# Kernel tuning notes

Hardware: AMD Instinct MI355X
Metric: run time of the kernel (lower is better)

Reference implementation:

```python
import jax, jax.numpy as jnp
import numpy as np

DT = 0.1  # fixed dt offset from init_kwargs


def setup_inputs() -> dict:
    key = jax.random.key(0)
    ks = jax.random.split(key, 8)
    B_, L, D, N = 4, 4096, 128, 16
    s = 1.0 / np.sqrt(D)
    # S4D-Real init: A_n = -(n+1), repeated over input_dim (random_init=False)
    A = jnp.broadcast_to(-(jnp.arange(N, dtype=jnp.float32) + 1.0), (D, N))
    return {
        "x": jax.random.normal(ks[0], (B_, L, D), dtype=jnp.float32),
        "A": A,
        "Wb": jax.random.uniform(ks[1], (N, D), minval=-s, maxval=s, dtype=jnp.float32),
        "bb": jax.random.uniform(ks[2], (N,), minval=-s, maxval=s, dtype=jnp.float32),
        "Wc": jax.random.uniform(ks[3], (N, D), minval=-s, maxval=s, dtype=jnp.float32),
        "bc": jax.random.uniform(ks[4], (N,), minval=-s, maxval=s, dtype=jnp.float32),
        "Wd": jax.random.uniform(ks[5], (1, D), minval=-s, maxval=s, dtype=jnp.float32),
        "bd": jax.random.uniform(ks[6], (1,), minval=-s, maxval=s, dtype=jnp.float32),
    }


def reference(x, A, Wb, bb, Wc, bc, Wd, bd):
    # x: [B, L, D]; A: [D, N]
    Bp = x @ Wb.T + bb                                   # [B, L, N]  (self.sb)
    C = x @ Wc.T + bc                                    # [B, L, N]  (self.sc)
    # DeltaNetwork: softplus(Linear(x)) + dt, repeated over input_dim
    delta = jax.nn.softplus(x @ Wd.T + bd) + DT          # [B, L, 1]
    delta = jnp.broadcast_to(delta, x.shape)             # [B, L, D]
    # discretize: A_bar = exp(dt*A); B_bar = (1 - exp(-dt*A)) * (dt x B)
    dA = delta[..., None] * A                            # [B, L, D, N]
    A_bar = jnp.exp(dA)
    Bx = (1.0 - jnp.exp(-dA)) * delta[..., None] * Bp[:, :, None, :] * x[..., None]  # B_bar * x_t

    def step(h, inp):
        A_t, Bx_t, C_t = inp                             # [B,D,N],[B,D,N],[B,N]
        h = A_t * h + Bx_t
        y_t = jnp.sum(h * C_t[:, None, :], axis=-1)      # [B, D]
        return h, y_t

    h0 = jnp.zeros((x.shape[0], x.shape[2], A.shape[1]), x.dtype)
    _, y = jax.lax.scan(
        step, h0,
        (A_bar.transpose(1, 0, 2, 3), Bx.transpose(1, 0, 2, 3), C.transpose(1, 0, 2)),
    )
    return y.transpose(1, 0, 2)                          # [B, L, D]
```

## Files before the change

kernel.cpp:

```cpp
#include <hip/hip_runtime.h>
#include <math.h>

#define B_ 4
#define L_ 4096
#define D_ 128
#define N_ 16
#define DT_ 0.1f
#define CHUNK_ 32
#define NC_ 128

#define HL_OFF 0
#define H0_OFF 1048576
#define P_OFF  2097152
#define W_OFF  2105344

__global__ __launch_bounds__(256) void kA_fused(const float* __restrict__ x,
                                                const float* __restrict__ A,
                                                const float* __restrict__ Wb,
                                                const float* __restrict__ bb,
                                                const float* __restrict__ Wc,
                                                const float* __restrict__ bc,
                                                const float* __restrict__ Wd,
                                                const float* __restrict__ bd,
                                                float* __restrict__ ws,
                                                float* __restrict__ y) {
    __shared__ float xs[32][132];
    __shared__ float proj[32][34];
    __shared__ float delta_s[32];
    __shared__ float Ssum[32];
    __shared__ float a_s[32][16];
    __shared__ float c_s[32][16];
    __shared__ float C_s[32][16];

    const int t = threadIdx.x;
    const int blk = blockIdx.x;
    const int b = blk >> 7;
    const int c = blk & 127;
    const int l0 = c * CHUNK_;

    const float4* xg = (const float4*)(x + ((size_t)b * L_ + l0) * 128);
#pragma unroll
    for (int i = t; i < 1024; i += 256) {
        float4 v = xg[i];
        int r = i >> 5, c4 = (i & 31) << 2;
        xs[r][c4] = v.x; xs[r][c4 + 1] = v.y;
        xs[r][c4 + 2] = v.z; xs[r][c4 + 3] = v.w;
    }
    __syncthreads();

    {
        const int wv = t >> 6;
        const int lane = t & 63;
        const int r = lane & 31;
        const int oh = lane >> 5;
        const int ob = wv * 8 + oh * 4;
        const float* wp = (ob < 16) ? (Wb + (size_t)ob * 128)
                                    : (Wc + (size_t)(ob - 16) * 128);
        const bool do32 = (wv == 0) && (oh == 0);
        float a0 = 0.f, a1 = 0.f, a2 = 0.f, a3 = 0.f, ad = 0.f;
#pragma unroll 4
        for (int k4 = 0; k4 < 32; ++k4) {
            float4 xv = *(const float4*)&xs[r][k4 * 4];
            float4 w0 = *(const float4*)(wp + k4 * 4);
            float4 w1 = *(const float4*)(wp + 128 + k4 * 4);
            float4 w2 = *(const float4*)(wp + 256 + k4 * 4);
            float4 w3 = *(const float4*)(wp + 384 + k4 * 4);
            a0 = fmaf(xv.x, w0.x, a0); a0 = fmaf(xv.y, w0.y, a0);
            a0 = fmaf(xv.z, w0.z, a0); a0 = fmaf(xv.w, w0.w, a0);
            a1 = fmaf(xv.x, w1.x, a1); a1 = fmaf(xv.y, w1.y, a1);
            a1 = fmaf(xv.z, w1.z, a1); a1 = fmaf(xv.w, w1.w, a1);
            a2 = fmaf(xv.x, w2.x, a2); a2 = fmaf(xv.y, w2.y, a2);
            a2 = fmaf(xv.z, w2.z, a2); a2 = fmaf(xv.w, w2.w, a2);
            a3 = fmaf(xv.x, w3.x, a3); a3 = fmaf(xv.y, w3.y, a3);
            a3 = fmaf(xv.z, w3.z, a3); a3 = fmaf(xv.w, w3.w, a3);
            if (do32) {
                float4 w4 = *(const float4*)(Wd + k4 * 4);
                ad = fmaf(xv.x, w4.x, ad); ad = fmaf(xv.y, w4.y, ad);
                ad = fmaf(xv.z, w4.z, ad); ad = fmaf(xv.w, w4.w, ad);
            }
        }
        proj[r][ob] = a0; proj[r][ob + 1] = a1;
        proj[r][ob + 2] = a2; proj[r][ob + 3] = a3;
        if (do32) proj[r][32] = ad;
    }
    __syncthreads();

    if (t < 32) {
        float z = proj[t][32] + bd[0];
        float sp = fmaxf(z, 0.f) + log1pf(expf(-fabsf(z)));
        delta_s[t] = sp + DT_;
    }
    __syncthreads();
    if (t == 0) {
        float s = 0.f;
        for (int r = 0; r < 32; ++r) { s += delta_s[r]; Ssum[r] = s; }
    }
    __syncthreads();

    {
        float* wglob = ws + W_OFF + ((size_t)b * L_ + l0) * 16;
#pragma unroll
        for (int p = t; p < 512; p += 256) {
            int r = p >> 4, n = p & 15;
            float An = A[n];
            float delta = delta_s[r];
            float Bp = proj[r][n] + bb[n];
            float Cv = proj[r][16 + n] + bc[n];
            float dA = delta * An;
            a_s[r][n] = expf(dA);
            c_s[r][n] = (1.f - expf(-dA)) * delta * Bp;
            C_s[r][n] = Cv;
            wglob[p] = Cv * expf(An * Ssum[r]);
        }
        if (t < 16) {
            ws[P_OFF + (size_t)blk * 16 + t] = expf(A[t] * Ssum[31]);
        }
    }
    __syncthreads();

    const int dd = t >> 2;
    const int nq = t & 3;
    float h0v = 0.f, h1v = 0.f, h2v = 0.f, h3v = 0.f;
    float g0v = 0.f, g1v = 0.f, g2v = 0.f, g3v = 0.f;
    float* yout = y + ((size_t)b * L_ + l0) * 128;
#pragma unroll 4
    for (int tt = 0; tt < 32; ++tt) {
        float4 av = *(const float4*)&a_s[tt][nq * 4];
        float4 cv = *(const float4*)&c_s[tt][nq * 4];
        float4 Cv = *(const float4*)&C_s[tt][nq * 4];
        float x0 = xs[tt][dd];
        float x1 = xs[tt][dd + 64];
        h0v = fmaf(av.x, h0v, cv.x * x0);
        h1v = fmaf(av.y, h1v, cv.y * x0);
        h2v = fmaf(av.z, h2v, cv.z * x0);
        h3v = fmaf(av.w, h3v, cv.w * x0);
        g0v = fmaf(av.x, g0v, cv.x * x1);
        g1v = fmaf(av.y, g1v, cv.y * x1);
        g2v = fmaf(av.z, g2v, cv.z * x1);
        g3v = fmaf(av.w, g3v, cv.w * x1);
        float y0 = h0v * Cv.x;
        y0 = fmaf(h1v, Cv.y, y0); y0 = fmaf(h2v, Cv.z, y0); y0 = fmaf(h3v, Cv.w, y0);
        float y1 = g0v * Cv.x;
        y1 = fmaf(g1v, Cv.y, y1); y1 = fmaf(g2v, Cv.z, y1); y1 = fmaf(g3v, Cv.w, y1);
        y0 += __shfl_xor(y0, 1); y0 += __shfl_xor(y0, 2);
        y1 += __shfl_xor(y1, 1); y1 += __shfl_xor(y1, 2);
        if (nq == 0) {
            yout[tt * 128 + dd] = y0;
            yout[tt * 128 + dd + 64] = y1;
        }
    }
    float* hL = ws + HL_OFF + (size_t)blk * 2048;
    *(float4*)(hL + dd * 16 + nq * 4) = make_float4(h0v, h1v, h2v, h3v);
    *(float4*)(hL + (dd + 64) * 16 + nq * 4) = make_float4(g0v, g1v, g2v, g3v);
}

__global__ __launch_bounds__(256, 4) void kB_combine(float* __restrict__ ws) {
    const float* hL = ws + HL_OFF;
    const float* Pp = ws + P_OFF;
    float* h0 = ws + H0_OFF;
    const int tid = blockIdx.x * 256 + threadIdx.x;
    const int b = tid >> 11;
    const int dn = tid & 2047;
    const int n = tid & 15;

    const float* hp = hL + (size_t)b * NC_ * 2048 + dn;
    const float* pp = Pp + (size_t)b * NC_ * 16 + n;
    float* op = h0 + (size_t)b * NC_ * 2048 + dn;

    float h = 0.f;
    op[0] = 0.f;
#pragma unroll 8
    for (int c = 0; c < NC_ - 1; ++c) {
        float hl = hp[(size_t)c * 2048];
        float p  = pp[(size_t)c * 16];
        h = fmaf(p, h, hl);
        op[(size_t)(c + 1) * 2048] = h;
    }
}

__global__ __launch_bounds__(256, 4) void kC_update(const float* __restrict__ ws,
                                                    float* __restrict__ y) {
    __shared__ float w_s[32][16];
    const int blk = blockIdx.x;
    const int b = blk >> 7;
    const int c = blk & 127;
    const int t = threadIdx.x;

    if (t < 128) {
        float4 v = ((const float4*)(ws + W_OFF + ((size_t)b * L_ + c * CHUNK_) * 16))[t];
        int tt = t >> 2, n0 = (t & 3) << 2;
        w_s[tt][n0] = v.x; w_s[tt][n0 + 1] = v.y;
        w_s[tt][n0 + 2] = v.z; w_s[tt][n0 + 3] = v.w;
    }
    __syncthreads();

    const int d = t & 127;
    const int rh = t >> 7;
    const float* h0p = ws + H0_OFF + ((size_t)blk * 128 + d) * 16;
    const float4 ha = *(const float4*)h0p;
    const float4 hb = *(const float4*)(h0p + 4);
    const float4 hc = *(const float4*)(h0p + 8);
    const float4 hd = *(const float4*)(h0p + 12);

    float* yp = y + ((size_t)b * L_ + c * CHUNK_ + rh * 16) * 128 + d;
#pragma unroll
    for (int i = 0; i < 16; ++i) {
        const int tt = rh * 16 + i;
        float4 wa = *(const float4*)&w_s[tt][0];
        float4 wb4 = *(const float4*)&w_s[tt][4];
        float4 wc4 = *(const float4*)&w_s[tt][8];
        float4 wd4 = *(const float4*)&w_s[tt][12];
        float s = yp[i * 128];
        s = fmaf(wa.x, ha.x, s); s = fmaf(wa.y, ha.y, s);
        s = fmaf(wa.z, ha.z, s); s = fmaf(wa.w, ha.w, s);
        s = fmaf(wb4.x, hb.x, s); s = fmaf(wb4.y, hb.y, s);
        s = fmaf(wb4.z, hb.z, s); s = fmaf(wb4.w, hb.w, s);
        s = fmaf(wc4.x, hc.x, s); s = fmaf(wc4.y, hc.y, s);
        s = fmaf(wc4.z, hc.z, s); s = fmaf(wc4.w, hc.w, s);
        s = fmaf(wd4.x, hd.x, s); s = fmaf(wd4.y, hd.y, s);
        s = fmaf(wd4.z, hd.z, s); s = fmaf(wd4.w, hd.w, s);
        yp[i * 128] = s;
    }
}

extern "C" void kernel_launch(void* const* d_in, const int* in_sizes, int n_in,
                              void* d_out, int out_size, void* d_ws, size_t ws_size,
                              hipStream_t stream) {
    const float* x  = (const float*)d_in[0];
    const float* A  = (const float*)d_in[1];
    const float* Wb = (const float*)d_in[2];
    const float* bb = (const float*)d_in[3];
    const float* Wc = (const float*)d_in[4];
    const float* bc = (const float*)d_in[5];
    const float* Wd = (const float*)d_in[6];
    const float* bd = (const float*)d_in[7];
    float* ws = (float*)d_ws;
    float* y  = (float*)d_out;

    kA_fused<<<512, 256, 0, stream>>>(x, A, Wb, bb, Wc, bc, Wd, bd, ws, y);
    kB_combine<<<32, 256, 0, stream>>>(ws);
    kC_update<<<512, 256, 0, stream>>>(ws, y);
}
```

Measured before the change: 131.2 us.

## Fuse chunked scan into one kernel with inter-block flag sync

```diff
diff --git a/kernel.cpp b/kernel.cpp
--- a/kernel.cpp
+++ b/kernel.cpp
@@ -6,59 +6,56 @@
 #define D_ 128
 #define N_ 16
 #define DT_ 0.1f
-#define CHUNK_ 32
-#define NC_ 128
-
-#define HL_OFF 0
-#define H0_OFF 1048576
-#define P_OFF  2097152
-#define W_OFF  2105344
-
-__global__ __launch_bounds__(256) void kA_fused(const float* __restrict__ x,
-                                                const float* __restrict__ A,
-                                                const float* __restrict__ Wb,
-                                                const float* __restrict__ bb,
-                                                const float* __restrict__ Wc,
-                                                const float* __restrict__ bc,
-                                                const float* __restrict__ Wd,
-                                                const float* __restrict__ bd,
-                                                float* __restrict__ ws,
-                                                float* __restrict__ y) {
-    __shared__ float xs[32][132];
-    __shared__ float proj[32][34];
-    __shared__ float delta_s[32];
-    __shared__ float Ssum[32];
-    __shared__ float a_s[32][16];
-    __shared__ float c_s[32][16];
-    __shared__ float C_s[32][16];
+#define CH_ 64
+#define NCH_ 64
+#define MAGICF 0x5D5D5D5Du
+
+#define CF_OFF 0
+#define HL_OFF 786432
+#define PR_OFF 1310720
+#define FL_OFF 1314816
+
+__global__ __launch_bounds__(512, 2) void s6_fused(const float* __restrict__ x,
+                                                   const float* __restrict__ A,
+                                                   const float* __restrict__ Wb,
+                                                   const float* __restrict__ bb,
+                                                   const float* __restrict__ Wc,
+                                                   const float* __restrict__ bc,
+                                                   const float* __restrict__ Wd,
+                                                   const float* __restrict__ bd,
+                                                   float* __restrict__ ws,
+                                                   float* __restrict__ y) {
+    __shared__ float xs[64][132];
+    __shared__ float proj[64][36];
+    __shared__ float delta_s[64];
+    __shared__ float Ssum[64];
+    __shared__ float w_s[64][16];
+    __shared__ float ylocal[64][132];
+    __shared__ float h0s[128][20];
 
     const int t = threadIdx.x;
     const int blk = blockIdx.x;
-    const int b = blk >> 7;
-    const int c = blk & 127;
-    const int l0 = c * CHUNK_;
-
-    const float4* xg = (const float4*)(x + ((size_t)b * L_ + l0) * 128);
-#pragma unroll
-    for (int i = t; i < 1024; i += 256) {
+    const int b = blk >> 6;
+    const int c = blk & 63;
+    const size_t rowbase = (size_t)b * L_ + c * CH_;
+
+    const float4* xg = (const float4*)(x + rowbase * 128);
+#pragma unroll
+    for (int i = t; i < 2048; i += 512) {
         float4 v = xg[i];
-        int r = i >> 5, c4 = (i & 31) << 2;
-        xs[r][c4] = v.x; xs[r][c4 + 1] = v.y;
-        xs[r][c4 + 2] = v.z; xs[r][c4 + 3] = v.w;
+        int r = i >> 5, k4 = (i & 31) << 2;
+        xs[r][k4] = v.x; xs[r][k4 + 1] = v.y;
+        xs[r][k4 + 2] = v.z; xs[r][k4 + 3] = v.w;
     }
     __syncthreads();
 
     {
-        const int wv = t >> 6;
-        const int lane = t & 63;
-        const int r = lane & 31;
-        const int oh = lane >> 5;
-        const int ob = wv * 8 + oh * 4;
-        const float* wp = (ob < 16) ? (Wb + (size_t)ob * 128)
-                                    : (Wc + (size_t)(ob - 16) * 128);
-        const bool do32 = (wv == 0) && (oh == 0);
-        float a0 = 0.f, a1 = 0.f, a2 = 0.f, a3 = 0.f, ad = 0.f;
-#pragma unroll 4
+        const int q = t >> 6;
+        const int r = t & 63;
+        const float* wp = (q < 4) ? (Wb + (size_t)q * 4 * 128)
+                                  : (Wc + (size_t)(q - 4) * 4 * 128);
+        float a0 = 0.f, a1 = 0.f, a2 = 0.f, a3 = 0.f;
+#pragma unroll 8
         for (int k4 = 0; k4 < 32; ++k4) {
             float4 xv = *(const float4*)&xs[r][k4 * 4];
             float4 w0 = *(const float4*)(wp + k4 * 4);
@@ -73,153 +70,177 @@
             a2 = fmaf(xv.z, w2.z, a2); a2 = fmaf(xv.w, w2.w, a2);
             a3 = fmaf(xv.x, w3.x, a3); a3 = fmaf(xv.y, w3.y, a3);
             a3 = fmaf(xv.z, w3.z, a3); a3 = fmaf(xv.w, w3.w, a3);
-            if (do32) {
-                float4 w4 = *(const float4*)(Wd + k4 * 4);
-                ad = fmaf(xv.x, w4.x, ad); ad = fmaf(xv.y, w4.y, ad);
-                ad = fmaf(xv.z, w4.z, ad); ad = fmaf(xv.w, w4.w, ad);
+        }
+        proj[r][q * 4]     = a0;
+        proj[r][q * 4 + 1] = a1;
+        proj[r][q * 4 + 2] = a2;
+        proj[r][q * 4 + 3] = a3;
+        if (q == 0) {
+            float ad = 0.f;
+#pragma unroll 8
+            for (int k4 = 0; k4 < 32; ++k4) {
+                float4 xv = *(const float4*)&xs[r][k4 * 4];
+                float4 wv = *(const float4*)(Wd + k4 * 4);
+                ad = fmaf(xv.x, wv.x, ad); ad = fmaf(xv.y, wv.y, ad);
+                ad = fmaf(xv.z, wv.z, ad); ad = fmaf(xv.w, wv.w, ad);
             }
-        }
-        proj[r][ob] = a0; proj[r][ob + 1] = a1;
-        proj[r][ob + 2] = a2; proj[r][ob + 3] = a3;
-        if (do32) proj[r][32] = ad;
-    }
-    __syncthreads();
-
-    if (t < 32) {
+            proj[r][32] = ad;
+        }
+    }
+    __syncthreads();
+
+    if (t < 64) {
         float z = proj[t][32] + bd[0];
         float sp = fmaxf(z, 0.f) + log1pf(expf(-fabsf(z)));
-        delta_s[t] = sp + DT_;
-    }
-    __syncthreads();
+        float dl = sp + DT_;
+        delta_s[t] = dl;
+        float v = dl;
+#pragma unroll
+        for (int off = 1; off < 64; off <<= 1) {
+            float u = __shfl_up(v, off);
+            if (t >= off) v += u;
+        }
+        Ssum[t] = v;
+    }
+    __syncthreads();
+
+    float* cg = ws + CF_OFF + (size_t)blk * 3072;
+#pragma unroll
+    for (int p = t; p < 1024; p += 512) {
+        int r = p >> 4, n = p & 15;
+        float An = A[n];
+        float dl = delta_s[r];
+        float Bp = proj[r][n] + bb[n];
+        float Cv = proj[r][16 + n] + bc[n];
+        float dA = dl * An;
+        cg[r * 48 + n]      = expf(dA);
+        cg[r * 48 + 16 + n] = (1.f - expf(-dA)) * dl * Bp;
+        cg[r * 48 + 32 + n] = Cv;
+        w_s[r][n] = Cv * expf(An * Ssum[r]);
+    }
+    if (t < 16) ws[PR_OFF + (size_t)blk * 16 + t] = expf(A[t] * Ssum[63]);
+    __syncthreads();
+
+    if (t < 128) {
+        const int d = t;
+        float4 h0 = {0.f, 0.f, 0.f, 0.f}, h1 = {0.f, 0.f, 0.f, 0.f};
+        float4 h2 = {0.f, 0.f, 0.f, 0.f}, h3 = {0.f, 0.f, 0.f, 0.f};
+#pragma unroll 2
+        for (int tt = 0; tt < 64; ++tt) {
+            const float* ct = cg + tt * 48;
+            float4 a0 = *(const float4*)(ct);
+            float4 a1 = *(const float4*)(ct + 4);
+            float4 a2 = *(const float4*)(ct + 8);
+            float4 a3 = *(const float4*)(ct + 12);
+            float4 c0 = *(const float4*)(ct + 16);
+            float4 c1 = *(const float4*)(ct + 20);
+            float4 c2 = *(const float4*)(ct + 24);
+            float4 c3 = *(const float4*)(ct + 28);
+            float4 C0 = *(const float4*)(ct + 32);
+            float4 C1 = *(const float4*)(ct + 36);
+            float4 C2 = *(const float4*)(ct + 40);
+            float4 C3 = *(const float4*)(ct + 44);
+            float xv = xs[tt][d];
+            h0.x = fmaf(a0.x, h0.x, c0.x * xv);
+            h0.y = fmaf(a0.y, h0.y, c0.y * xv);
+            h0.z = fmaf(a0.z, h0.z, c0.z * xv);
+            h0.w = fmaf(a0.w, h0.w, c0.w * xv);
+            h1.x = fmaf(a1.x, h1.x, c1.x * xv);
+            h1.y = fmaf(a1.y, h1.y, c1.y * xv);
+            h1.z = fmaf(a1.z, h1.z, c1.z * xv);
+            h1.w = fmaf(a1.w, h1.w, c1.w * xv);
+            h2.x = fmaf(a2.x, h2.x, c2.x * xv);
+            h2.y = fmaf(a2.y, h2.y, c2.y * xv);
+            h2.z = fmaf(a2.z, h2.z, c2.z * xv);
+            h2.w = fmaf(a2.w, h2.w, c2.w * xv);
+            h3.x = fmaf(a3.x, h3.x, c3.x * xv);
+            h3.y = fmaf(a3.y, h3.y, c3.y * xv);
+            h3.z = fmaf(a3.z, h3.z, c3.z * xv);
+            h3.w = fmaf(a3.w, h3.w, c3.w * xv);
+            float yv = h0.x * C0.x;
+            yv = fmaf(h0.y, C0.y, yv); yv = fmaf(h0.z, C0.z, yv);
+            yv = fmaf(h0.w, C0.w, yv);
+            yv = fmaf(h1.x, C1.x, yv); yv = fmaf(h1.y, C1.y, yv);
+            yv = fmaf(h1.z, C1.z, yv); yv = fmaf(h1.w, C1.w, yv);
+            yv = fmaf(h2.x, C2.x, yv); yv = fmaf(h2.y, C2.y, yv);
+            yv = fmaf(h2.z, C2.z, yv); yv = fmaf(h2.w, C2.w, yv);
+            yv = fmaf(h3.x, C3.x, yv); yv = fmaf(h3.y, C3.y, yv);
+            yv = fmaf(h3.z, C3.z, yv); yv = fmaf(h3.w, C3.w, yv);
+            ylocal[tt][d] = yv;
+        }
+        float* hp = ws + HL_OFF + (size_t)blk * 2048 + d * 16;
+        *(float4*)(hp)      = h0;
+        *(float4*)(hp + 4)  = h1;
+        *(float4*)(hp + 8)  = h2;
+        *(float4*)(hp + 12) = h3;
+    }
+    __syncthreads();
+
+    unsigned* flg = (unsigned*)(ws + FL_OFF);
     if (t == 0) {
-        float s = 0.f;
-        for (int r = 0; r < 32; ++r) { s += delta_s[r]; Ssum[r] = s; }
-    }
-    __syncthreads();
+        __threadfence();
+        __hip_atomic_store(&flg[blk], MAGICF, __ATOMIC_RELEASE,
+                           __HIP_MEMORY_SCOPE_AGENT);
+    }
+
+    if (t < c) {
+        long iter = 0;
+        while (__hip_atomic_load(&flg[(b << 6) + t], __ATOMIC_ACQUIRE,
+                                 __HIP_MEMORY_SCOPE_AGENT) != MAGICF) {
+            __builtin_amdgcn_s_sleep(4);
+            if (++iter > 100000000L) break;
+        }
+    }
+    __syncthreads();
+    __threadfence();
 
     {
-        float* wglob = ws + W_OFF + ((size_t)b * L_ + l0) * 16;
-#pragma unroll
-        for (int p = t; p < 512; p += 256) {
-            int r = p >> 4, n = p & 15;
-            float An = A[n];
-            float delta = delta_s[r];
-            float Bp = proj[r][n] + bb[n];
-            float Cv = proj[r][16 + n] + bc[n];
-            float dA = delta * An;
-            a_s[r][n] = expf(dA);
-            c_s[r][n] = (1.f - expf(-dA)) * delta * Bp;
-            C_s[r][n] = Cv;
-            wglob[p] = Cv * expf(An * Ssum[r]);
-        }
-        if (t < 16) {
-            ws[P_OFF + (size_t)blk * 16 + t] = expf(A[t] * Ssum[31]);
-        }
-    }
-    __syncthreads();
-
-    const int dd = t >> 2;
-    const int nq = t & 3;
-    float h0v = 0.f, h1v = 0.f, h2v = 0.f, h3v = 0.f;
-    float g0v = 0.f, g1v = 0.f, g2v = 0.f, g3v = 0.f;
-    float* yout = y + ((size_t)b * L_ + l0) * 128;
+        const int d = t >> 2, nq = t & 3;
+        float4 s = {0.f, 0.f, 0.f, 0.f};
+        const float* hb = ws + HL_OFF + ((size_t)(b << 6)) * 2048 + d * 16 + nq * 4;
+        const float* pb = ws + PR_OFF + ((size_t)(b << 6)) * 16 + nq * 4;
 #pragma unroll 4
-    for (int tt = 0; tt < 32; ++tt) {
-        float4 av = *(const float4*)&a_s[tt][nq * 4];
-        float4 cv = *(const float4*)&c_s[tt][nq * 4];
-        float4 Cv = *(const float4*)&C_s[tt][nq * 4];
-        float x0 = xs[tt][dd];
-        float x1 = xs[tt][dd + 64];
-        h0v = fmaf(av.x, h0v, cv.x * x0);
-        h1v = fmaf(av.y, h1v, cv.y * x0);
-        h2v = fmaf(av.z, h2v, cv.z * x0);
-        h3v = fmaf(av.w, h3v, cv.w * x0);
-        g0v = fmaf(av.x, g0v, cv.x * x1);
-        g1v = fmaf(av.y, g1v, cv.y * x1);
-        g2v = fmaf(av.z, g2v, cv.z * x1);
-        g3v = fmaf(av.w, g3v, cv.w * x1);
-        float y0 = h0v * Cv.x;
-        y0 = fmaf(h1v, Cv.y, y0); y0 = fmaf(h2v, Cv.z, y0); y0 = fmaf(h3v, Cv.w, y0);
-        float y1 = g0v * Cv.x;
-        y1 = fmaf(g1v, Cv.y, y1); y1 = fmaf(g2v, Cv.z, y1); y1 = fmaf(g3v, Cv.w, y1);
-        y0 += __shfl_xor(y0, 1); y0 += __shfl_xor(y0, 2);
-        y1 += __shfl_xor(y1, 1); y1 += __shfl_xor(y1, 2);
-        if (nq == 0) {
-            yout[tt * 128 + dd] = y0;
-            yout[tt * 128 + dd + 64] = y1;
-        }
-    }
-    float* hL = ws + HL_OFF + (size_t)blk * 2048;
-    *(float4*)(hL + dd * 16 + nq * 4) = make_float4(h0v, h1v, h2v, h3v);
-    *(float4*)(hL + (dd + 64) * 16 + nq * 4) = make_float4(g0v, g1v, g2v, g3v);
-}
-
-__global__ __launch_bounds__(256, 4) void kB_combine(float* __restrict__ ws) {
-    const float* hL = ws + HL_OFF;
-    const float* Pp = ws + P_OFF;
-    float* h0 = ws + H0_OFF;
-    const int tid = blockIdx.x * 256 + threadIdx.x;
-    const int b = tid >> 11;
-    const int dn = tid & 2047;
-    const int n = tid & 15;
-
-    const float* hp = hL + (size_t)b * NC_ * 2048 + dn;
-    const float* pp = Pp + (size_t)b * NC_ * 16 + n;
-    float* op = h0 + (size_t)b * NC_ * 2048 + dn;
-
-    float h = 0.f;
-    op[0] = 0.f;
-#pragma unroll 8
-    for (int c = 0; c < NC_ - 1; ++c) {
-        float hl = hp[(size_t)c * 2048];
-        float p  = pp[(size_t)c * 16];
-        h = fmaf(p, h, hl);
-        op[(size_t)(c + 1) * 2048] = h;
-    }
-}
-
-__global__ __launch_bounds__(256, 4) void kC_update(const float* __restrict__ ws,
-                                                    float* __restrict__ y) {
-    __shared__ float w_s[32][16];
-    const int blk = blockIdx.x;
-    const int b = blk >> 7;
-    const int c = blk & 127;
-    const int t = threadIdx.x;
-
-    if (t < 128) {
-        float4 v = ((const float4*)(ws + W_OFF + ((size_t)b * L_ + c * CHUNK_) * 16))[t];
-        int tt = t >> 2, n0 = (t & 3) << 2;
-        w_s[tt][n0] = v.x; w_s[tt][n0 + 1] = v.y;
-        w_s[tt][n0 + 2] = v.z; w_s[tt][n0 + 3] = v.w;
-    }
-    __syncthreads();
-
-    const int d = t & 127;
-    const int rh = t >> 7;
-    const float* h0p = ws + H0_OFF + ((size_t)blk * 128 + d) * 16;
-    const float4 ha = *(const float4*)h0p;
-    const float4 hb = *(const float4*)(h0p + 4);
-    const float4 hc = *(const float4*)(h0p + 8);
-    const float4 hd = *(const float4*)(h0p + 12);
-
-    float* yp = y + ((size_t)b * L_ + c * CHUNK_ + rh * 16) * 128 + d;
-#pragma unroll
-    for (int i = 0; i < 16; ++i) {
-        const int tt = rh * 16 + i;
-        float4 wa = *(const float4*)&w_s[tt][0];
-        float4 wb4 = *(const float4*)&w_s[tt][4];
-        float4 wc4 = *(const float4*)&w_s[tt][8];
-        float4 wd4 = *(const float4*)&w_s[tt][12];
-        float s = yp[i * 128];
-        s = fmaf(wa.x, ha.x, s); s = fmaf(wa.y, ha.y, s);
-        s = fmaf(wa.z, ha.z, s); s = fmaf(wa.w, ha.w, s);
-        s = fmaf(wb4.x, hb.x, s); s = fmaf(wb4.y, hb.y, s);
-        s = fmaf(wb4.z, hb.z, s); s = fmaf(wb4.w, hb.w, s);
-        s = fmaf(wc4.x, hc.x, s); s = fmaf(wc4.y, hc.y, s);
-        s = fmaf(wc4.z, hc.z, s); s = fmaf(wc4.w, hc.w, s);
-        s = fmaf(wd4.x, hd.x, s); s = fmaf(wd4.y, hd.y, s);
-        s = fmaf(wd4.z, hd.z, s); s = fmaf(wd4.w, hd.w, s);
-        yp[i * 128] = s;
+        for (int j = 0; j < c; ++j) {
+            float4 hl = *(const float4*)(hb + (size_t)j * 2048);
+            float4 p  = *(const float4*)(pb + (size_t)j * 16);
+            s.x = fmaf(p.x, s.x, hl.x);
+            s.y = fmaf(p.y, s.y, hl.y);
+            s.z = fmaf(p.z, s.z, hl.z);
+            s.w = fmaf(p.w, s.w, hl.w);
+        }
+        h0s[d][nq * 4]     = s.x;
+        h0s[d][nq * 4 + 1] = s.y;
+        h0s[d][nq * 4 + 2] = s.z;
+        h0s[d][nq * 4 + 3] = s.w;
+    }
+    __syncthreads();
+
+    {
+        const int d2 = t & 127;
+        const int rg = t >> 7;
+        float4 ha = *(const float4*)&h0s[d2][0];
+        float4 hb4 = *(const float4*)&h0s[d2][4];
+        float4 hc4 = *(const float4*)&h0s[d2][8];
+        float4 hd4 = *(const float4*)&h0s[d2][12];
+        float* yo = y + (rowbase + rg * 16) * 128 + d2;
+#pragma unroll
+        for (int i = 0; i < 16; ++i) {
+            int tt = rg * 16 + i;
+            float4 wa = *(const float4*)&w_s[tt][0];
+            float4 wb4 = *(const float4*)&w_s[tt][4];
+            float4 wc4 = *(const float4*)&w_s[tt][8];
+            float4 wd4 = *(const float4*)&w_s[tt][12];
+            float s = ylocal[tt][d2];
+            s = fmaf(wa.x, ha.x, s);  s = fmaf(wa.y, ha.y, s);
+            s = fmaf(wa.z, ha.z, s);  s = fmaf(wa.w, ha.w, s);
+            s = fmaf(wb4.x, hb4.x, s); s = fmaf(wb4.y, hb4.y, s);
+            s = fmaf(wb4.z, hb4.z, s); s = fmaf(wb4.w, hb4.w, s);
+            s = fmaf(wc4.x, hc4.x, s); s = fmaf(wc4.y, hc4.y, s);
+            s = fmaf(wc4.z, hc4.z, s); s = fmaf(wc4.w, hc4.w, s);
+            s = fmaf(wd4.x, hd4.x, s); s = fmaf(wd4.y, hd4.y, s);
+            s = fmaf(wd4.z, hd4.z, s); s = fmaf(wd4.w, hd4.w, s);
+            yo[i * 128] = s;
+        }
     }
 }
 
@@ -237,7 +258,5 @@
     float* ws = (float*)d_ws;
     float* y  = (float*)d_out;
 
-    kA_fused<<<512, 256, 0, stream>>>(x, A, Wb, bb, Wc, bc, Wd, bd, ws, y);
-    kB_combine<<<32, 256, 0, stream>>>(ws);
-    kC_update<<<512, 256, 0, stream>>>(ws, y);
+    s6_fused<<<256, 512, 0, stream>>>(x, A, Wb, bb, Wc, bc, Wd, bd, ws, y);
 }
```

Result: slower. 158.3 us (+20.7%).
